# Performance work log

Hardware: AMD Instinct MI355X
Metric: run time of the kernel (lower is better)

The kernel has to match this reference:

```python
import jax, jax.numpy as jnp
import numpy as np

N_USERS = 100000
N_ITEMS = 50000
EMB_DIM = 64
N_LAYERS = 2
N_INTENTS = 128
N_EDGES = 4000000
N_NODES = N_USERS + N_ITEMS


def setup_inputs() -> dict:
    key = jax.random.key(0)
    k1, k2, k3, k4, k5 = jax.random.split(key, 5)
    return {
        "user_emb": 0.1 * jax.random.normal(k1, (N_USERS, EMB_DIM), dtype=jnp.float32),
        "item_emb": 0.1 * jax.random.normal(k2, (N_ITEMS, EMB_DIM), dtype=jnp.float32),
        "intents": jax.random.normal(k3, (EMB_DIM, N_INTENTS), dtype=jnp.float32) * (2.0 / (EMB_DIM + N_INTENTS)) ** 0.5,
        "h_idx": jax.random.randint(k4, (N_EDGES,), 0, N_NODES, dtype=jnp.int64)
        if jax.config.jax_enable_x64 else jax.random.randint(k4, (N_EDGES,), 0, N_NODES, dtype=jnp.int32),
        "t_idx": jax.random.randint(k5, (N_EDGES,), 0, N_NODES, dtype=jnp.int32),
    }


def _spmm(h_idx, t_idx, g_vals, x):
    # y[h] += g_vals * x[t]  (sparse matrix @ dense, COO form)
    gathered = x[t_idx] * g_vals[:, None]  # [E, D]
    return jax.ops.segment_sum(gathered, h_idx, num_segments=N_NODES)


def reference(user_emb, item_emb, intents, h_idx, t_idx):
    # --- _cal_sparse_adj: G = D^{-1/2} A D^{-1/2}, A values are ones ---
    deg = jax.ops.segment_sum(jnp.ones_like(h_idx, dtype=user_emb.dtype), h_idx,
                              num_segments=N_NODES)
    d_inv_sqrt = jnp.where(deg > 0, jax.lax.rsqrt(jnp.maximum(deg, 1e-12)), 0.0)
    g_vals = d_inv_sqrt[h_idx] * d_inv_sqrt[t_idx]  # [E]

    # --- multi-layer propagation with intent-aware embeddings ---
    embs = jnp.concatenate([user_emb, item_emb], axis=0)  # [N, D]
    all_embs = [embs]
    for _ in range(N_LAYERS):
        gnn_embs = _spmm(h_idx, t_idx, g_vals, embs)  # [N, D]
        # intent projection: softmax over intents, reconstruct in emb space
        u, it = embs[:N_USERS], embs[N_USERS:]
        u_int = jax.nn.softmax(u @ intents, axis=1) @ intents.T      # [n_users, D]
        i_int = jax.nn.softmax(it @ intents, axis=1) @ intents.T     # [n_items, D]
        int_embs = jnp.concatenate([u_int, i_int], axis=0)
        embs = gnn_embs + int_embs
        all_embs.append(embs)
    out = jnp.sum(jnp.stack(all_embs, axis=1), axis=1) / len(all_embs)  # mean over layers
    return out
```

## Files before the change

kernel.cpp:

```cpp
#include <hip/hip_runtime.h>
#include <math.h>

#define N_USERS 100000
#define N_ITEMS 50000
#define N_NODES 150000
#define EMB 64
#define NI 128
#define NUM_EDGES 4000000
#define NPAD 150016
#define NB 586
#define BSTRIDE 8192
#define ETILE 4096
#define EGRID ((NUM_EDGES + ETILE - 1) / ETILE)
#define NTILES (N_NODES / 16)
#define SBLK ((NTILES + 3) / 4)

typedef __attribute__((ext_vector_type(8))) short bf16x8;
typedef __attribute__((ext_vector_type(4))) float f32x4;

__device__ __forceinline__ unsigned short f2bf(float f) {
    unsigned int u = __float_as_uint(f);
    u += 0x7FFFu + ((u >> 16) & 1u);
    return (unsigned short)(u >> 16);
}
__device__ __forceinline__ float bflo(unsigned int u) { return __uint_as_float(u << 16); }
__device__ __forceinline__ float bfhi(unsigned int u) { return __uint_as_float(u & 0xFFFF0000u); }


__global__ __launch_bounds__(256) void bucket_scatter(const int* __restrict__ h,
                                                      const int* __restrict__ t,
                                                      int* __restrict__ gcur,
                                                      unsigned int* __restrict__ ebuf) {
    __shared__ int lc[NB];
    __shared__ int lbase[NB];
    __shared__ int lcur[NB];
    int tid = threadIdx.x;
    for (int i = tid; i < NB; i += 256) lc[i] = 0;
    __syncthreads();
    int base = blockIdx.x * ETILE;
#pragma unroll
    for (int k = 0; k < ETILE / 256; ++k) {
        int idx = base + k * 256 + tid;
        if (idx < NUM_EDGES) atomicAdd(&lc[h[idx] >> 8], 1);
    }
    __syncthreads();
    for (int i = tid; i < NB; i += 256) {
        int c = lc[i];
        lbase[i] = c ? (i * BSTRIDE + atomicAdd(&gcur[i], c)) : 0;
        lcur[i] = 0;
    }
    __syncthreads();
#pragma unroll
    for (int k = 0; k < ETILE / 256; ++k) {
        int idx = base + k * 256 + tid;
        if (idx < NUM_EDGES) {
            int hh = h[idx], tt = t[idx];
            int b = hh >> 8;
            int p = lbase[b] + atomicAdd(&lcur[b], 1);
            int lim = b * BSTRIDE + BSTRIDE - 1;
            p = (p <= lim) ? p : lim;
            ebuf[p] = ((unsigned int)(hh & 255) << 18) | (unsigned int)tt;
        }
    }
}


__global__ __launch_bounds__(256) void bucket_csr(const int* __restrict__ gcur,
                                                  unsigned int* __restrict__ ebuf,
                                                  int2* __restrict__ rmeta,
                                                  float* __restrict__ dinv) {
    __shared__ unsigned int in_s[BSTRIDE];
    __shared__ unsigned int out_s[BSTRIDE];
    __shared__ int cnt_s[256];
    __shared__ int base_s[256];
    __shared__ int sc[256];
    int b = blockIdx.x, tid = threadIdx.x;
    int s = b * BSTRIDE;
    int n = gcur[b];
    if (n > BSTRIDE) n = BSTRIDE;

    for (int i = tid; i < n; i += 256) in_s[i] = ebuf[s + i];
    cnt_s[tid] = 0;
    __syncthreads();
    for (int i = tid; i < n; i += 256) atomicAdd(&cnt_s[in_s[i] >> 18], 1);
    __syncthreads();

    int c = cnt_s[tid];
    sc[tid] = c;
    __syncthreads();
    for (int off = 1; off < 256; off <<= 1) {
        int tv = (tid >= off) ? sc[tid - off] : 0;
        __syncthreads();
        sc[tid] += tv;
        __syncthreads();
    }
    int excl = sc[tid] - c;
    base_s[tid] = excl;
    int node = (b << 8) + tid;
    rmeta[node] = make_int2(s + excl, c);
    dinv[node] = (c > 0) ? rsqrtf((float)c) : 0.0f;
    cnt_s[tid] = 0;
    __syncthreads();

    for (int i = tid; i < n; i += 256) {
        unsigned int q = in_s[i];
        int hl = (int)(q >> 18);
        int p = base_s[hl] + atomicAdd(&cnt_s[hl], 1);
        out_s[p] = q & 0x3FFFFu;
    }
    __syncthreads();
    for (int i = tid; i < n; i += 256) ebuf[s + i] = out_s[i];
}


__global__ void init_kernel(const float4* __restrict__ ue4, const float4* __restrict__ ie4,
                            uint2* __restrict__ ebf4, float4* __restrict__ out4) {
    int i = blockIdx.x * blockDim.x + threadIdx.x;
    const int uelems = N_USERS * EMB / 4;
    const int total  = N_NODES * EMB / 4;
    if (i < total) {
        float4 v = (i < uelems) ? ue4[i] : ie4[i - uelems];
        out4[i] = v;
        unsigned int p0 = ((unsigned int)f2bf(v.y) << 16) | f2bf(v.x);
        unsigned int p1 = ((unsigned int)f2bf(v.w) << 16) | f2bf(v.z);
        ebf4[i] = make_uint2(p0, p1);
    }
}


__global__ __launch_bounds__(256) void wconv(const float* __restrict__ W,
                                             unsigned short* __restrict__ Wt,
                                             unsigned short* __restrict__ W2b) {
    int i = blockIdx.x * 256 + threadIdx.x;
    if (i < EMB * NI) {
        int d = i >> 7, c = i & 127;
        unsigned short b = f2bf(W[i]);
        W2b[i] = b;
        Wt[c * EMB + d] = b;
    }
}


__global__ __launch_bounds__(256, 7) void spmm_intent(const int2* __restrict__ rmeta,
                                                      const unsigned int* __restrict__ col,
                                                      const float* __restrict__ dinv,
                                                      const unsigned short* __restrict__ ebf,
                                                      unsigned short* __restrict__ ebfout,
                                                      const unsigned short* __restrict__ Wt,
                                                      const unsigned short* __restrict__ W2b,
                                                      float* __restrict__ acc, float scale) {
    __shared__ __align__(16) float UPool[4][1408];

    int tid = threadIdx.x;
    int wid = tid >> 6, lane = tid & 63;
    int q = lane >> 4, c = lane & 15;
    int qq = lane >> 3, cc = lane & 7;
    int tile = blockIdx.x * 4 + wid;
    if (tile >= NTILES) return;
    int rowbase = tile << 4;
    float* fw = &UPool[wid][0];
    unsigned short* pw = (unsigned short*)&UPool[wid][1088];

#pragma unroll 1
    for (int half = 0; half < 2; ++half) {
        int row = rowbase + half * 8 + qq;
        int2 rm = rmeta[row];
        int s = rm.x, deg = rm.y;
        float dr = dinv[row];
        int dm = deg;
        dm = max(dm, __shfl_xor(dm, 8));
        dm = max(dm, __shfl_xor(dm, 16));
        dm = max(dm, __shfl_xor(dm, 32));
        dm = __builtin_amdgcn_readfirstlane(dm);

        float a0 = 0.f, a1 = 0.f, a2 = 0.f, a3 = 0.f;
        float a4 = 0.f, a5 = 0.f, a6 = 0.f, a7 = 0.f;
        int last = s + ((deg > 0) ? (deg - 1) : 0);
        int ce0 = min((int)col[s], N_NODES - 1);
        int ce1 = min((int)col[min(s + 1, last)], N_NODES - 1);
        int ce2 = min((int)col[min(s + 2, last)], N_NODES - 1);
        int ce3 = min((int)col[min(s + 3, last)], N_NODES - 1);
        float g0 = dinv[ce0], g1 = dinv[ce1], g2 = dinv[ce2], g3 = dinv[ce3];
        const unsigned short* eb = ebf + (cc << 3);
        for (int it = 0; it < dm; it += 4) {
            float gu0 = (it < deg) ? g0 : 0.f;
            float gu1 = (it + 1 < deg) ? g1 : 0.f;
            float gu2 = (it + 2 < deg) ? g2 : 0.f;
            float gu3 = (it + 3 < deg) ? g3 : 0.f;
            uint4 u0 = *(const uint4*)(eb + ((size_t)ce0 << 6));
            uint4 u1 = *(const uint4*)(eb + ((size_t)ce1 << 6));
            uint4 u2 = *(const uint4*)(eb + ((size_t)ce2 << 6));
            uint4 u3 = *(const uint4*)(eb + ((size_t)ce3 << 6));
            int p0 = min(s + it + 4, last), p1 = min(s + it + 5, last);
            int p2 = min(s + it + 6, last), p3 = min(s + it + 7, last);
            ce0 = min((int)col[p0], N_NODES - 1);
            ce1 = min((int)col[p1], N_NODES - 1);
            ce2 = min((int)col[p2], N_NODES - 1);
            ce3 = min((int)col[p3], N_NODES - 1);
            g0 = dinv[ce0]; g1 = dinv[ce1]; g2 = dinv[ce2]; g3 = dinv[ce3];
            a0 = fmaf(gu0, bflo(u0.x), a0); a1 = fmaf(gu0, bfhi(u0.x), a1);
            a2 = fmaf(gu0, bflo(u0.y), a2); a3 = fmaf(gu0, bfhi(u0.y), a3);
            a4 = fmaf(gu0, bflo(u0.z), a4); a5 = fmaf(gu0, bfhi(u0.z), a5);
            a6 = fmaf(gu0, bflo(u0.w), a6); a7 = fmaf(gu0, bfhi(u0.w), a7);
            a0 = fmaf(gu1, bflo(u1.x), a0); a1 = fmaf(gu1, bfhi(u1.x), a1);
            a2 = fmaf(gu1, bflo(u1.y), a2); a3 = fmaf(gu1, bfhi(u1.y), a3);
            a4 = fmaf(gu1, bflo(u1.z), a4); a5 = fmaf(gu1, bfhi(u1.z), a5);
            a6 = fmaf(gu1, bflo(u1.w), a6); a7 = fmaf(gu1, bfhi(u1.w), a7);
            a0 = fmaf(gu2, bflo(u2.x), a0); a1 = fmaf(gu2, bfhi(u2.x), a1);
            a2 = fmaf(gu2, bflo(u2.y), a2); a3 = fmaf(gu2, bfhi(u2.y), a3);
            a4 = fmaf(gu2, bflo(u2.z), a4); a5 = fmaf(gu2, bfhi(u2.z), a5);
            a6 = fmaf(gu2, bflo(u2.w), a6); a7 = fmaf(gu2, bfhi(u2.w), a7);
            a0 = fmaf(gu3, bflo(u3.x), a0); a1 = fmaf(gu3, bfhi(u3.x), a1);
            a2 = fmaf(gu3, bflo(u3.y), a2); a3 = fmaf(gu3, bfhi(u3.y), a3);
            a4 = fmaf(gu3, bflo(u3.z), a4); a5 = fmaf(gu3, bfhi(u3.z), a5);
            a6 = fmaf(gu3, bflo(u3.w), a6); a7 = fmaf(gu3, bfhi(u3.w), a7);
        }
        int fb = (half * 8 + qq) * 68 + (cc << 3);
        fw[fb + 0] = a0 * dr; fw[fb + 1] = a1 * dr;
        fw[fb + 2] = a2 * dr; fw[fb + 3] = a3 * dr;
        fw[fb + 4] = a4 * dr; fw[fb + 5] = a5 * dr;
        fw[fb + 6] = a6 * dr; fw[fb + 7] = a7 * dr;
    }

    const unsigned short* erow = ebf + ((size_t)(rowbase + c) << 6);
    bf16x8 A0 = *(const bf16x8*)(erow + (q << 3));
    bf16x8 A1 = *(const bf16x8*)(erow + 32 + (q << 3));
    f32x4 S[8];
#pragma unroll
    for (int t = 0; t < 8; ++t) {
        bf16x8 B0 = *(const bf16x8*)&Wt[(16 * t + c) * EMB + (q << 3)];
        bf16x8 B1 = *(const bf16x8*)&Wt[(16 * t + c) * EMB + 32 + (q << 3)];
        f32x4 z = {0.f, 0.f, 0.f, 0.f};
        z = __builtin_amdgcn_mfma_f32_16x16x32_bf16(A0, B0, z, 0, 0, 0);
        S[t] = __builtin_amdgcn_mfma_f32_16x16x32_bf16(A1, B1, z, 0, 0, 0);
    }

#pragma unroll
    for (int r = 0; r < 4; ++r) {
        float m = S[0][r];
#pragma unroll
        for (int t = 1; t < 8; ++t) m = fmaxf(m, S[t][r]);
        m = fmaxf(m, __shfl_xor(m, 1)); m = fmaxf(m, __shfl_xor(m, 2));
        m = fmaxf(m, __shfl_xor(m, 4)); m = fmaxf(m, __shfl_xor(m, 8));
        float sum = 0.f;
#pragma unroll
        for (int t = 0; t < 8; ++t) { float ex = __expf(S[t][r] - m); S[t][r] = ex; sum += ex; }
        sum += __shfl_xor(sum, 1); sum += __shfl_xor(sum, 2);
        sum += __shfl_xor(sum, 4); sum += __shfl_xor(sum, 8);
        float inv = 1.0f / sum;
#pragma unroll
        for (int t = 0; t < 8; ++t) S[t][r] *= inv;
    }

    f32x4 O0 = {0.f, 0.f, 0.f, 0.f}, O1 = O0, O2 = O0, O3 = O0;
#pragma unroll
    for (int s2 = 0; s2 < 4; ++s2) {
#pragma unroll
        for (int h2 = 0; h2 < 2; ++h2) {
            int t = 2 * s2 + h2;
#pragma unroll
            for (int r = 0; r < 4; ++r) {
                float p = S[t][r];
                unsigned short b = f2bf(p);
                pw[(4 * q + r) * 40 + (h2 << 4) + c] = b;
                S[t][r] = p - bflo((unsigned int)b);
            }
        }
        bf16x8 Pf = *(const bf16x8*)&pw[c * 40 + (q << 3)];
        {
            bf16x8 Bf0 = *(const bf16x8*)&W2b[(c) * NI + (s2 << 5) + (q << 3)];
            bf16x8 Bf1 = *(const bf16x8*)&W2b[(16 + c) * NI + (s2 << 5) + (q << 3)];
            O0 = __builtin_amdgcn_mfma_f32_16x16x32_bf16(Pf, Bf0, O0, 0, 0, 0);
            O1 = __builtin_amdgcn_mfma_f32_16x16x32_bf16(Pf, Bf1, O1, 0, 0, 0);
            bf16x8 Bf2 = *(const bf16x8*)&W2b[(32 + c) * NI + (s2 << 5) + (q << 3)];
            bf16x8 Bf3 = *(const bf16x8*)&W2b[(48 + c) * NI + (s2 << 5) + (q << 3)];
            O2 = __builtin_amdgcn_mfma_f32_16x16x32_bf16(Pf, Bf2, O2, 0, 0, 0);
            O3 = __builtin_amdgcn_mfma_f32_16x16x32_bf16(Pf, Bf3, O3, 0, 0, 0);
        }
#pragma unroll
        for (int h2 = 0; h2 < 2; ++h2) {
            int t = 2 * s2 + h2;
#pragma unroll
            for (int r = 0; r < 4; ++r)
                pw[(4 * q + r) * 40 + (h2 << 4) + c] = f2bf(S[t][r]);
        }
        bf16x8 Pl = *(const bf16x8*)&pw[c * 40 + (q << 3)];
        {
            bf16x8 Bf0 = *(const bf16x8*)&W2b[(c) * NI + (s2 << 5) + (q << 3)];
            bf16x8 Bf1 = *(const bf16x8*)&W2b[(16 + c) * NI + (s2 << 5) + (q << 3)];
            O0 = __builtin_amdgcn_mfma_f32_16x16x32_bf16(Pl, Bf0, O0, 0, 0, 0);
            O1 = __builtin_amdgcn_mfma_f32_16x16x32_bf16(Pl, Bf1, O1, 0, 0, 0);
            bf16x8 Bf2 = *(const bf16x8*)&W2b[(32 + c) * NI + (s2 << 5) + (q << 3)];
            bf16x8 Bf3 = *(const bf16x8*)&W2b[(48 + c) * NI + (s2 << 5) + (q << 3)];
            O2 = __builtin_amdgcn_mfma_f32_16x16x32_bf16(Pl, Bf2, O2, 0, 0, 0);
            O3 = __builtin_amdgcn_mfma_f32_16x16x32_bf16(Pl, Bf3, O3, 0, 0, 0);
        }
    }

    asm volatile("" ::: "memory");

#pragma unroll
    for (int r = 0; r < 4; ++r) {
        int rl = 4 * q + r;
        const float* gr = &fw[rl * 68];
        size_t rbase = ((size_t)(rowbase + rl) << 6);
        float nv0 = gr[c]      + O0[r];
        float nv1 = gr[16 + c] + O1[r];
        float nv2 = gr[32 + c] + O2[r];
        float nv3 = gr[48 + c] + O3[r];
        ebfout[rbase + c]      = f2bf(nv0);
        ebfout[rbase + 16 + c] = f2bf(nv1);
        ebfout[rbase + 32 + c] = f2bf(nv2);
        ebfout[rbase + 48 + c] = f2bf(nv3);
        acc[rbase + c]      = (acc[rbase + c]      + nv0) * scale;
        acc[rbase + 16 + c] = (acc[rbase + 16 + c] + nv1) * scale;
        acc[rbase + 32 + c] = (acc[rbase + 32 + c] + nv2) * scale;
        acc[rbase + 48 + c] = (acc[rbase + 48 + c] + nv3) * scale;
    }
}


extern "C" void kernel_launch(void* const* d_in, const int* in_sizes, int n_in,
                              void* d_out, int out_size, void* d_ws, size_t ws_size,
                              hipStream_t stream) {
    const float* ue = (const float*)d_in[0];
    const float* ie = (const float*)d_in[1];
    const float* W  = (const float*)d_in[2];
    const int*   h  = (const int*)d_in[3];
    const int*   t  = (const int*)d_in[4];
    float* out = (float*)d_out;

    int*            gcur  = (int*)d_ws;
    int2*           rmeta = (int2*)(gcur + 1024);
    float*          dinv  = (float*)(rmeta + NPAD);
    unsigned int*   ebuf  = (unsigned int*)(dinv + NPAD);
    unsigned short* Wt    = (unsigned short*)(ebuf + NB * BSTRIDE);
    unsigned short* W2b   = Wt + EMB * NI;
    unsigned short* ebfA  = W2b + EMB * NI;
    unsigned short* ebfB  = ebfA + (size_t)NPAD * EMB;

    hipMemsetAsync(gcur, 0, NB * sizeof(int), stream);
    bucket_scatter<<<EGRID, 256, 0, stream>>>(h, t, gcur, ebuf);
    bucket_csr<<<NB, 256, 0, stream>>>(gcur, ebuf, rmeta, dinv);
    init_kernel<<<(N_NODES * EMB / 4 + 255) / 256, 256, 0, stream>>>(
        (const float4*)ue, (const float4*)ie, (uint2*)ebfA, (float4*)out);
    wconv<<<(EMB * NI + 255) / 256, 256, 0, stream>>>(W, Wt, W2b);

    const unsigned int* col = ebuf;
    spmm_intent<<<SBLK, 256, 0, stream>>>(rmeta, col, dinv, ebfA, ebfB, Wt, W2b, out, 1.0f);
    spmm_intent<<<SBLK, 256, 0, stream>>>(rmeta, col, dinv, ebfB, ebfA, Wt, W2b, out, 1.0f / 3.0f);
}
```

Measured before the change: 485.5 us.

## Deepen SpMM gather prefetch, vectorize epilogue stores, widen bucket kernels

The SpMM gather loop now prefetches one extra group of column indices, dinv values and embedding rows, so the loads for the next four edges are issued before the current FMAs. The output epilogue stages results through shared memory and writes bf16 and fp32 rows with 16-byte vector stores instead of scattered scalar stores. The bucket kernels move to 512 threads with a larger edge tile, and the CSR kernel writes sorted columns directly to global memory instead of staging them in a second shared buffer. Occupancy for spmm_intent is lowered to leave room for the extra prefetch registers.

```diff
diff --git a/kernel.cpp b/kernel.cpp
--- a/kernel.cpp
+++ b/kernel.cpp
@@ -10,7 +10,7 @@
 #define NPAD 150016
 #define NB 586
 #define BSTRIDE 8192
-#define ETILE 4096
+#define ETILE 8192
 #define EGRID ((NUM_EDGES + ETILE - 1) / ETILE)
 #define NTILES (N_NODES / 16)
 #define SBLK ((NTILES + 3) / 4)
@@ -25,9 +25,13 @@
 }
 __device__ __forceinline__ float bflo(unsigned int u) { return __uint_as_float(u << 16); }
 __device__ __forceinline__ float bfhi(unsigned int u) { return __uint_as_float(u & 0xFFFF0000u); }
-
-
-__global__ __launch_bounds__(256) void bucket_scatter(const int* __restrict__ h,
+__device__ __forceinline__ int cl_idx(unsigned int v) {
+    int x = (int)(v & 0x3FFFFu);
+    return (x < N_NODES) ? x : (N_NODES - 1);
+}
+
+
+__global__ __launch_bounds__(512) void bucket_scatter(const int* __restrict__ h,
                                                       const int* __restrict__ t,
                                                       int* __restrict__ gcur,
                                                       unsigned int* __restrict__ ebuf) {
@@ -35,24 +39,24 @@
     __shared__ int lbase[NB];
     __shared__ int lcur[NB];
     int tid = threadIdx.x;
-    for (int i = tid; i < NB; i += 256) lc[i] = 0;
+    for (int i = tid; i < NB; i += 512) lc[i] = 0;
     __syncthreads();
     int base = blockIdx.x * ETILE;
 #pragma unroll
-    for (int k = 0; k < ETILE / 256; ++k) {
-        int idx = base + k * 256 + tid;
+    for (int k = 0; k < ETILE / 512; ++k) {
+        int idx = base + k * 512 + tid;
         if (idx < NUM_EDGES) atomicAdd(&lc[h[idx] >> 8], 1);
     }
     __syncthreads();
-    for (int i = tid; i < NB; i += 256) {
+    for (int i = tid; i < NB; i += 512) {
         int c = lc[i];
         lbase[i] = c ? (i * BSTRIDE + atomicAdd(&gcur[i], c)) : 0;
         lcur[i] = 0;
     }
     __syncthreads();
 #pragma unroll
-    for (int k = 0; k < ETILE / 256; ++k) {
-        int idx = base + k * 256 + tid;
+    for (int k = 0; k < ETILE / 512; ++k) {
+        int idx = base + k * 512 + tid;
         if (idx < NUM_EDGES) {
             int hh = h[idx], tt = t[idx];
             int b = hh >> 8;
@@ -65,12 +69,11 @@
 }
 
 
-__global__ __launch_bounds__(256) void bucket_csr(const int* __restrict__ gcur,
+__global__ __launch_bounds__(512) void bucket_csr(const int* __restrict__ gcur,
                                                   unsigned int* __restrict__ ebuf,
                                                   int2* __restrict__ rmeta,
                                                   float* __restrict__ dinv) {
     __shared__ unsigned int in_s[BSTRIDE];
-    __shared__ unsigned int out_s[BSTRIDE];
     __shared__ int cnt_s[256];
     __shared__ int base_s[256];
     __shared__ int sc[256];
@@ -79,37 +82,38 @@
     int n = gcur[b];
     if (n > BSTRIDE) n = BSTRIDE;
 
-    for (int i = tid; i < n; i += 256) in_s[i] = ebuf[s + i];
-    cnt_s[tid] = 0;
-    __syncthreads();
-    for (int i = tid; i < n; i += 256) atomicAdd(&cnt_s[in_s[i] >> 18], 1);
-    __syncthreads();
-
-    int c = cnt_s[tid];
-    sc[tid] = c;
+    for (int i = tid; i < n; i += 512) in_s[i] = ebuf[s + i];
+    if (tid < 256) cnt_s[tid] = 0;
+    __syncthreads();
+    for (int i = tid; i < n; i += 512) atomicAdd(&cnt_s[in_s[i] >> 18], 1);
+    __syncthreads();
+
+    int c = 0;
+    if (tid < 256) { c = cnt_s[tid]; sc[tid] = c; }
     __syncthreads();
     for (int off = 1; off < 256; off <<= 1) {
-        int tv = (tid >= off) ? sc[tid - off] : 0;
+        int tv = 0;
+        if (tid < 256 && tid >= off) tv = sc[tid - off];
         __syncthreads();
-        sc[tid] += tv;
+        if (tid < 256 && tid >= off) sc[tid] += tv;
         __syncthreads();
     }
-    int excl = sc[tid] - c;
-    base_s[tid] = excl;
-    int node = (b << 8) + tid;
-    rmeta[node] = make_int2(s + excl, c);
-    dinv[node] = (c > 0) ? rsqrtf((float)c) : 0.0f;
-    cnt_s[tid] = 0;
-    __syncthreads();
-
-    for (int i = tid; i < n; i += 256) {
-        unsigned int q = in_s[i];
-        int hl = (int)(q >> 18);
+    if (tid < 256) {
+        int excl = sc[tid] - c;
+        base_s[tid] = excl;
+        int node = (b << 8) + tid;
+        rmeta[node] = make_int2(s + excl, c);
+        dinv[node] = (c > 0) ? rsqrtf((float)c) : 0.0f;
+        cnt_s[tid] = 0;
+    }
+    __syncthreads();
+
+    for (int i = tid; i < n; i += 512) {
+        unsigned int qv = in_s[i];
+        int hl = (int)(qv >> 18);
         int p = base_s[hl] + atomicAdd(&cnt_s[hl], 1);
-        out_s[p] = q & 0x3FFFFu;
-    }
-    __syncthreads();
-    for (int i = tid; i < n; i += 256) ebuf[s + i] = out_s[i];
+        ebuf[s + p] = qv & 0x3FFFFu;
+    }
 }
 
 
@@ -141,7 +145,7 @@
 }
 
 
-__global__ __launch_bounds__(256, 7) void spmm_intent(const int2* __restrict__ rmeta,
+__global__ __launch_bounds__(256, 6) void spmm_intent(const int2* __restrict__ rmeta,
                                                       const unsigned int* __restrict__ col,
                                                       const float* __restrict__ dinv,
                                                       const unsigned short* __restrict__ ebf,
@@ -176,28 +180,36 @@
         float a0 = 0.f, a1 = 0.f, a2 = 0.f, a3 = 0.f;
         float a4 = 0.f, a5 = 0.f, a6 = 0.f, a7 = 0.f;
         int last = s + ((deg > 0) ? (deg - 1) : 0);
-        int ce0 = min((int)col[s], N_NODES - 1);
-        int ce1 = min((int)col[min(s + 1, last)], N_NODES - 1);
-        int ce2 = min((int)col[min(s + 2, last)], N_NODES - 1);
-        int ce3 = min((int)col[min(s + 3, last)], N_NODES - 1);
+        const unsigned short* eb = ebf + (cc << 3);
+
+        int ce0 = cl_idx(col[s]);
+        int ce1 = cl_idx(col[min(s + 1, last)]);
+        int ce2 = cl_idx(col[min(s + 2, last)]);
+        int ce3 = cl_idx(col[min(s + 3, last)]);
         float g0 = dinv[ce0], g1 = dinv[ce1], g2 = dinv[ce2], g3 = dinv[ce3];
-        const unsigned short* eb = ebf + (cc << 3);
+        uint4 u0 = *(const uint4*)(eb + ((size_t)ce0 << 6));
+        uint4 u1 = *(const uint4*)(eb + ((size_t)ce1 << 6));
+        uint4 u2 = *(const uint4*)(eb + ((size_t)ce2 << 6));
+        uint4 u3 = *(const uint4*)(eb + ((size_t)ce3 << 6));
+        int nc0 = cl_idx(col[min(s + 4, last)]);
+        int nc1 = cl_idx(col[min(s + 5, last)]);
+        int nc2 = cl_idx(col[min(s + 6, last)]);
+        int nc3 = cl_idx(col[min(s + 7, last)]);
+
         for (int it = 0; it < dm; it += 4) {
-            float gu0 = (it < deg) ? g0 : 0.f;
+            int f0 = cl_idx(col[min(s + it + 8, last)]);
+            int f1 = cl_idx(col[min(s + it + 9, last)]);
+            int f2 = cl_idx(col[min(s + it + 10, last)]);
+            int f3 = cl_idx(col[min(s + it + 11, last)]);
+            float h0 = dinv[nc0], h1 = dinv[nc1], h2 = dinv[nc2], h3 = dinv[nc3];
+            uint4 v0 = *(const uint4*)(eb + ((size_t)nc0 << 6));
+            uint4 v1 = *(const uint4*)(eb + ((size_t)nc1 << 6));
+            uint4 v2 = *(const uint4*)(eb + ((size_t)nc2 << 6));
+            uint4 v3 = *(const uint4*)(eb + ((size_t)nc3 << 6));
+            float gu0 = (it     < deg) ? g0 : 0.f;
             float gu1 = (it + 1 < deg) ? g1 : 0.f;
             float gu2 = (it + 2 < deg) ? g2 : 0.f;
             float gu3 = (it + 3 < deg) ? g3 : 0.f;
-            uint4 u0 = *(const uint4*)(eb + ((size_t)ce0 << 6));
-            uint4 u1 = *(const uint4*)(eb + ((size_t)ce1 << 6));
-            uint4 u2 = *(const uint4*)(eb + ((size_t)ce2 << 6));
-            uint4 u3 = *(const uint4*)(eb + ((size_t)ce3 << 6));
-            int p0 = min(s + it + 4, last), p1 = min(s + it + 5, last);
-            int p2 = min(s + it + 6, last), p3 = min(s + it + 7, last);
-            ce0 = min((int)col[p0], N_NODES - 1);
-            ce1 = min((int)col[p1], N_NODES - 1);
-            ce2 = min((int)col[p2], N_NODES - 1);
-            ce3 = min((int)col[p3], N_NODES - 1);
-            g0 = dinv[ce0]; g1 = dinv[ce1]; g2 = dinv[ce2]; g3 = dinv[ce3];
             a0 = fmaf(gu0, bflo(u0.x), a0); a1 = fmaf(gu0, bfhi(u0.x), a1);
             a2 = fmaf(gu0, bflo(u0.y), a2); a3 = fmaf(gu0, bfhi(u0.y), a3);
             a4 = fmaf(gu0, bflo(u0.z), a4); a5 = fmaf(gu0, bfhi(u0.z), a5);
@@ -214,6 +226,9 @@
             a2 = fmaf(gu3, bflo(u3.y), a2); a3 = fmaf(gu3, bfhi(u3.y), a3);
             a4 = fmaf(gu3, bflo(u3.z), a4); a5 = fmaf(gu3, bfhi(u3.z), a5);
             a6 = fmaf(gu3, bflo(u3.w), a6); a7 = fmaf(gu3, bfhi(u3.w), a7);
+            u0 = v0; u1 = v1; u2 = v2; u3 = v3;
+            g0 = h0; g1 = h1; g2 = h2; g3 = h3;
+            nc0 = f0; nc1 = f1; nc2 = f2; nc3 = f3;
         }
         int fb = (half * 8 + qq) * 68 + (cc << 3);
         fw[fb + 0] = a0 * dr; fw[fb + 1] = a1 * dr;
@@ -302,20 +317,43 @@
 #pragma unroll
     for (int r = 0; r < 4; ++r) {
         int rl = 4 * q + r;
-        const float* gr = &fw[rl * 68];
-        size_t rbase = ((size_t)(rowbase + rl) << 6);
-        float nv0 = gr[c]      + O0[r];
-        float nv1 = gr[16 + c] + O1[r];
-        float nv2 = gr[32 + c] + O2[r];
-        float nv3 = gr[48 + c] + O3[r];
-        ebfout[rbase + c]      = f2bf(nv0);
-        ebfout[rbase + 16 + c] = f2bf(nv1);
-        ebfout[rbase + 32 + c] = f2bf(nv2);
-        ebfout[rbase + 48 + c] = f2bf(nv3);
-        acc[rbase + c]      = (acc[rbase + c]      + nv0) * scale;
-        acc[rbase + 16 + c] = (acc[rbase + 16 + c] + nv1) * scale;
-        acc[rbase + 32 + c] = (acc[rbase + 32 + c] + nv2) * scale;
-        acc[rbase + 48 + c] = (acc[rbase + 48 + c] + nv3) * scale;
+        float* gr = &fw[rl * 68];
+        gr[c]      += O0[r];
+        gr[16 + c] += O1[r];
+        gr[32 + c] += O2[r];
+        gr[48 + c] += O3[r];
+    }
+
+    {
+        int j = lane >> 2, sg = lane & 3;
+        const float* gr = &fw[j * 68 + (sg << 4)];
+        float4 x0 = *(const float4*)&gr[0];
+        float4 x1 = *(const float4*)&gr[4];
+        float4 x2 = *(const float4*)&gr[8];
+        float4 x3 = *(const float4*)&gr[12];
+        size_t base = ((size_t)(rowbase + j) << 6) + (sg << 4);
+        uint4 w0, w1;
+        w0.x = (unsigned int)f2bf(x0.x) | ((unsigned int)f2bf(x0.y) << 16);
+        w0.y = (unsigned int)f2bf(x0.z) | ((unsigned int)f2bf(x0.w) << 16);
+        w0.z = (unsigned int)f2bf(x1.x) | ((unsigned int)f2bf(x1.y) << 16);
+        w0.w = (unsigned int)f2bf(x1.z) | ((unsigned int)f2bf(x1.w) << 16);
+        w1.x = (unsigned int)f2bf(x2.x) | ((unsigned int)f2bf(x2.y) << 16);
+        w1.y = (unsigned int)f2bf(x2.z) | ((unsigned int)f2bf(x2.w) << 16);
+        w1.z = (unsigned int)f2bf(x3.x) | ((unsigned int)f2bf(x3.y) << 16);
+        w1.w = (unsigned int)f2bf(x3.z) | ((unsigned int)f2bf(x3.w) << 16);
+        *(uint4*)(ebfout + base) = w0;
+        *(uint4*)(ebfout + base + 8) = w1;
+        float4* ap = (float4*)(acc + base);
+        float4 b0 = ap[0], b1 = ap[1], b2 = ap[2], b3 = ap[3];
+        b0.x = (b0.x + x0.x) * scale; b0.y = (b0.y + x0.y) * scale;
+        b0.z = (b0.z + x0.z) * scale; b0.w = (b0.w + x0.w) * scale;
+        b1.x = (b1.x + x1.x) * scale; b1.y = (b1.y + x1.y) * scale;
+        b1.z = (b1.z + x1.z) * scale; b1.w = (b1.w + x1.w) * scale;
+        b2.x = (b2.x + x2.x) * scale; b2.y = (b2.y + x2.y) * scale;
+        b2.z = (b2.z + x2.z) * scale; b2.w = (b2.w + x2.w) * scale;
+        b3.x = (b3.x + x3.x) * scale; b3.y = (b3.y + x3.y) * scale;
+        b3.z = (b3.z + x3.z) * scale; b3.w = (b3.w + x3.w) * scale;
+        ap[0] = b0; ap[1] = b1; ap[2] = b2; ap[3] = b3;
     }
 }
 
@@ -340,8 +378,8 @@
     unsigned short* ebfB  = ebfA + (size_t)NPAD * EMB;
 
     hipMemsetAsync(gcur, 0, NB * sizeof(int), stream);
-    bucket_scatter<<<EGRID, 256, 0, stream>>>(h, t, gcur, ebuf);
-    bucket_csr<<<NB, 256, 0, stream>>>(gcur, ebuf, rmeta, dinv);
+    bucket_scatter<<<EGRID, 512, 0, stream>>>(h, t, gcur, ebuf);
+    bucket_csr<<<NB, 512, 0, stream>>>(gcur, ebuf, rmeta, dinv);
     init_kernel<<<(N_NODES * EMB / 4 + 255) / 256, 256, 0, stream>>>(
         (const float4*)ue, (const float4*)ie, (uint2*)ebfA, (float4*)out);
     wconv<<<(EMB * NI + 255) / 256, 256, 0, stream>>>(W, Wt, W2b);
```

Measured after the change: 453.2 us. 1.07x faster.
